# Optimization experiments

Hardware: AMD Instinct MI355X
Metric: run time of the kernel (lower is better)

Reference implementation:

```python
import jax, jax.numpy as jnp
import numpy as np

N = 65536      # total nodes (64 graphs x 1024 nodes)
E = 1048576    # total edges
B = 64         # graphs in the batch
H = 128        # in_dim == hidden_dim
HEAD = 4
EPS = 1e-5


def setup_inputs() -> dict:
    key = jax.random.key(0)
    ks = jax.random.split(key, 16)
    s = 0.02
    return {
        "h": jax.random.normal(ks[0], (N, H), jnp.float32),
        "inter_f": jax.random.normal(ks[1], (B, H), jnp.float32),
        "gamma1": jnp.ones((H,), jnp.float32), "beta1": jnp.zeros((H,), jnp.float32),
        "W1": jax.random.normal(ks[2], (H, H), jnp.float32) * s, "b1": jnp.zeros((H,), jnp.float32),
        "gamma2": jnp.ones((H,), jnp.float32), "beta2": jnp.zeros((H,), jnp.float32),
        "W2": jax.random.normal(ks[3], (H, H), jnp.float32) * s, "b2": jnp.zeros((H,), jnp.float32),
        "Wq": jax.random.normal(ks[4], (HEAD, H, H), jnp.float32) * s,
        "Wk": jax.random.normal(ks[5], (HEAD, H, H), jnp.float32) * s,
        "Wv": jax.random.normal(ks[6], (HEAD, H, H), jnp.float32) * s,
        "Wc": jax.random.normal(ks[7], (HEAD * H, H), jnp.float32) * s,
        "ln_g": jnp.ones((H,), jnp.float32), "ln_b": jnp.zeros((H,), jnp.float32),
        "Wf1": jax.random.normal(ks[8], (H, 2 * H), jnp.float32) * s, "bf1": jnp.zeros((2 * H,), jnp.float32),
        "Wf2": jax.random.normal(ks[9], (2 * H, H), jnp.float32) * s, "bf2": jnp.zeros((H,), jnp.float32),
        "src": jax.random.randint(ks[10], (E,), 0, N, jnp.int32),
        "dst": jax.random.randint(ks[11], (E,), 0, N, jnp.int32),
        "graph_id": (jnp.arange(N) // (N // B)).astype(jnp.int32),
    }


def _bn(x, g, b):
    # BatchNorm1d (training-mode batch statistics, biased var)
    m = x.mean(0)
    v = jnp.mean((x - m) ** 2, 0)
    return (x - m) * jax.lax.rsqrt(v + EPS) * g + b


def _ln(x, g, b):
    m = x.mean(-1, keepdims=True)
    v = jnp.mean((x - m) ** 2, -1, keepdims=True)
    return (x - m) * jax.lax.rsqrt(v + EPS) * g + b


def _gconv(x, W, b, src, dst):
    # dgl GraphConv, norm='both': D_out^{-1/2} gather -> scatter-add -> D_in^{-1/2}, then W, b
    ones_e = jnp.ones((E,), x.dtype)
    dout = jnp.maximum(jax.ops.segment_sum(ones_e, src, num_segments=N), 1.0)
    din = jnp.maximum(jax.ops.segment_sum(ones_e, dst, num_segments=N), 1.0)
    msg = (x * jax.lax.rsqrt(dout)[:, None])[src]            # [E, H] gather
    agg = jax.ops.segment_sum(msg, dst, num_segments=N)      # [N, H] scatter-add
    agg = agg * jax.lax.rsqrt(din)[:, None]
    return agg @ W + b


def _forward(h, inter_f, gamma1, beta1, W1, b1, gamma2, beta2, W2, b2,
             Wq, Wk, Wv, Wc, ln_g, ln_b, Wf1, bf1, Wf2, bf2, src, dst, graph_id):
    # init pooling (mean_nodes)
    counts = jax.ops.segment_sum(jnp.ones((N,), h.dtype), graph_id, num_segments=B)
    init_avg_h = jax.ops.segment_sum(h, graph_id, num_segments=B) / counts[:, None]

    # two residual GraphConv blocks (dropout is identity at inference)
    h1 = h + jax.nn.relu(_gconv(_bn(h, gamma1, beta1), W1, b1, src, dst))
    h2 = h1 + jax.nn.relu(_gconv(_bn(h1, gamma2, beta2), W2, b2, src, dst))

    # broadcast_nodes(inter_f)
    inter_h = inter_f[graph_id]                               # [N, H]

    # transformer_block: per-head q/k/v, per-node scalar att, per-graph segment softmax
    q = jnp.einsum('nd,hdo->hno', h2, Wq)
    k = jnp.einsum('nd,hdo->hno', inter_h, Wk)
    v = jnp.einsum('nd,hdo->hno', h2, Wv)
    att = jnp.sum(q * k, axis=-1) / jnp.sqrt(jnp.float32(1280.0))   # [HEAD, N]
    mx = jax.vmap(lambda a: jax.ops.segment_max(a, graph_id, num_segments=B))(att)  # [HEAD, B]
    e = jnp.exp(att - mx[:, graph_id])
    ssum = jax.vmap(lambda a: jax.ops.segment_sum(a, graph_id, num_segments=B))(e)
    alpha = e / ssum[:, graph_id]                             # segment softmax per head
    tp = v * alpha[..., None]                                 # [HEAD, N, H]
    mo = tp.transpose(1, 0, 2).reshape(N, HEAD * H) @ Wc      # concat heads + project

    x1 = _ln(mo + h2, ln_g, ln_b)
    x2 = _ln(jax.nn.relu(x1 @ Wf1 + bf1) @ Wf2 + bf2 + x1, ln_g, ln_b)

    readout = jax.ops.segment_sum(x2, graph_id, num_segments=B)     # sum_nodes
    return readout, init_avg_h


def reference(h, inter_f, gamma1, beta1, W1, b1, gamma2, beta2, W2, b2,
              Wq, Wk, Wv, Wc, ln_g, ln_b, Wf1, bf1, Wf2, bf2, src, dst, graph_id):
    return _forward(h, inter_f, gamma1, beta1, W1, b1, gamma2, beta2, W2, b2,
                    Wq, Wk, Wv, Wc, ln_g, ln_b, Wf1, bf1, Wf2, bf2, src, dst, graph_id)
```

## Files before the change

kernel.cpp:

```cpp
#include <hip/hip_runtime.h>

#define NN 65536
#define NE 1048576
#define NB 64
#define HD 128
#define HD2 256
#define NHEAD 4
#define NPG 1024
#define BEPS 1e-5f
#define BM 64
#define ESTRIDE 20480

typedef short bf16x8s __attribute__((ext_vector_type(8)));
typedef float f32x4 __attribute__((ext_vector_type(4)));
#define MFMA16(a,b,c) __builtin_amdgcn_mfma_f32_16x16x32_bf16(a,b,c,0,0,0)

__device__ __forceinline__ unsigned short f2bf(float f) {
    union { float f; unsigned int u; } x{f};
    unsigned int r = x.u + 0x7FFFu + ((x.u >> 16) & 1u);
    return (unsigned short)(r >> 16);
}
__device__ __forceinline__ float b2f(unsigned short s) {
    union { unsigned int u; float f; } x{((unsigned int)s) << 16};
    return x.f;
}

__global__ __launch_bounds__(1024) void k_prep_pool(const int* __restrict__ src, const int* __restrict__ dst,
                                                    int* __restrict__ gcurD, int* __restrict__ gcurS,
                                                    unsigned int* __restrict__ dbuck, unsigned short* __restrict__ sbuck,
                                                    const float* __restrict__ h,
                                                    float* __restrict__ psum, float* __restrict__ psq) {
    const int t = threadIdx.x;
    if (blockIdx.x < 64) {
        __shared__ int cntD[64], cntS[64], baseD[64], baseS[64];
        if (t < 64) { cntD[t] = 0; cntS[t] = 0; }
        __syncthreads();
        const int e0 = blockIdx.x * 16384;
        int sv[16], dv[16];
        #pragma unroll
        for (int j = 0; j < 16; ++j) {
            int e = e0 + j * 1024 + t;
            sv[j] = src[e]; dv[j] = dst[e];
            atomicAdd(&cntD[dv[j] >> 10], 1);
            atomicAdd(&cntS[sv[j] >> 10], 1);
        }
        __syncthreads();
        if (t < 64) baseD[t] = atomicAdd(&gcurD[t * 32], cntD[t]);
        else if (t < 128) baseS[t - 64] = atomicAdd(&gcurS[(t - 64) * 32], cntS[t - 64]);
        __syncthreads();
        if (t < 64) { cntD[t] = 0; cntS[t] = 0; }
        __syncthreads();
        #pragma unroll
        for (int j = 0; j < 16; ++j) {
            int gd = dv[j] >> 10;
            int slot = baseD[gd] + atomicAdd(&cntD[gd], 1);
            if (slot < ESTRIDE)
                dbuck[gd * ESTRIDE + slot] = (unsigned)(dv[j] & 1023) | ((unsigned)sv[j] << 10);
            int gs = sv[j] >> 10;
            int slot2 = baseS[gs] + atomicAdd(&cntS[gs], 1);
            if (slot2 < ESTRIDE)
                sbuck[gs * ESTRIDE + slot2] = (unsigned short)(sv[j] & 1023);
        }
    } else {
        __shared__ float ls[1024], lq[1024];
        const int bb = blockIdx.x - 64;
        const int r0 = bb * 256;
        const int c = t & 127, strip8 = t >> 7;
        float s = 0.f, sq = 0.f;
        for (int i = 0; i < 32; ++i) {
            float v = h[(size_t)(r0 + strip8 * 32 + i) * HD + c];
            s += v; sq += v * v;
        }
        ls[t] = s; lq[t] = sq;
        __syncthreads();
        if (t < 128) {
            float ss = 0.f, qq = 0.f;
            #pragma unroll
            for (int k = 0; k < 8; ++k) { ss += ls[t + k * 128]; qq += lq[t + k * 128]; }
            psum[bb * HD + t] = ss;
            psq[bb * HD + t]  = qq;
        }
    }
}

__global__ __launch_bounds__(1024) void k_prep2(const int* __restrict__ gcurD, const int* __restrict__ gcurS,
                                                const unsigned int* __restrict__ dbuck,
                                                const unsigned short* __restrict__ sbuck,
                                                float* __restrict__ din_r, float* __restrict__ dout_r,
                                                int* __restrict__ beg, int* __restrict__ endv,
                                                unsigned short* __restrict__ elist) {
    __shared__ int hist[1024];
    __shared__ int pre[1024];
    const int t = threadIdx.x;
    const int b = blockIdx.x;
    if (b < 64) {
        const int g = b;
        const int n = min(gcurD[g * 32], ESTRIDE);
        const unsigned int* pd = dbuck + g * ESTRIDE;
        hist[t] = 0;
        __syncthreads();
        for (int i = t; i < n; i += 1024) atomicAdd(&hist[pd[i] & 1023], 1);
        __syncthreads();
        const int cnt = hist[t];
        din_r[g * 1024 + t] = rsqrtf((float)max(cnt, 1));
        int x = cnt; pre[t] = x;
        __syncthreads();
        #pragma unroll
        for (int off = 1; off < 1024; off <<= 1) {
            int v = (t >= off) ? pre[t - off] : 0;
            __syncthreads();
            x += v; pre[t] = x;
            __syncthreads();
        }
        const int excl = x - cnt;
        beg[g * 1024 + t]  = g * ESTRIDE + excl;
        endv[g * 1024 + t] = g * ESTRIDE + excl + cnt;
        __syncthreads();
        hist[t] = excl; pre[t] = 0;
        __syncthreads();
        for (int i = t; i < n; i += 1024) {
            unsigned int w = pd[i];
            int dl = w & 1023;
            int r = atomicAdd(&pre[dl], 1);
            elist[g * ESTRIDE + hist[dl] + r] = (unsigned short)(w >> 10);
        }
    } else {
        const int g = b - 64;
        const int m = min(gcurS[g * 32], ESTRIDE);
        const unsigned short* ps = sbuck + g * ESTRIDE;
        hist[t] = 0;
        __syncthreads();
        for (int i = t; i < m; i += 1024) atomicAdd(&hist[ps[i]], 1);
        __syncthreads();
        dout_r[g * 1024 + t] = rsqrtf((float)max(hist[t], 1));
    }
}

__global__ __launch_bounds__(256) void k_sd(const int* __restrict__ beg, const int* __restrict__ endv,
                                            const unsigned short* __restrict__ elist,
                                            const float* __restrict__ dout_r, float* __restrict__ sd) {
    const int node = blockIdx.x * 256 + threadIdx.x;
    const int b0 = beg[node], e0 = endv[node];
    float s = 0.f;
    for (int i = b0; i < e0; ++i) s += dout_r[elist[i]];
    sd[node] = s;
}

__global__ __launch_bounds__(256) void k_pack(const float* __restrict__ x, const float* __restrict__ dout_r,
                                              unsigned short* __restrict__ xr) {
    int idx = blockIdx.x * 256 + threadIdx.x;
    int node = idx >> 4;
    int c8 = (idx & 15) * 8;
    float dr = dout_r[node];
    float4 v0 = *(const float4*)(x + (size_t)node * HD + c8);
    float4 v1 = *(const float4*)(x + (size_t)node * HD + c8 + 4);
    union { uint4 v; unsigned short u[8]; } pk;
    pk.u[0] = f2bf(v0.x * dr); pk.u[1] = f2bf(v0.y * dr);
    pk.u[2] = f2bf(v0.z * dr); pk.u[3] = f2bf(v0.w * dr);
    pk.u[4] = f2bf(v1.x * dr); pk.u[5] = f2bf(v1.y * dr);
    pk.u[6] = f2bf(v1.z * dr); pk.u[7] = f2bf(v1.w * dr);
    *(uint4*)(xr + (size_t)node * HD + c8) = pk.v;
}

__device__ __forceinline__ void dev_prepW(int idx, const float* __restrict__ W,
                                          unsigned short* __restrict__ frag, int O) {
    int l = idx & 63, tt = idx >> 6;
    int ot = O >> 4;
    int c = tt % ot, ks = tt / ot;
    int q = l >> 4, m = l & 15;
    const float* wp = W + (size_t)(ks * 32 + q * 8) * O + c * 16 + m;
    union { uint4 v; unsigned short u[8]; } pk;
    #pragma unroll
    for (int j = 0; j < 8; ++j) pk.u[j] = f2bf(wp[(size_t)j * O]);
    *(uint4*)(frag + (size_t)idx * 8) = pk.v;
}

__global__ __launch_bounds__(256) void k_wprep(const float* __restrict__ W1, const float* __restrict__ W2,
                                               const float* __restrict__ Wf1, const float* __restrict__ Wf2,
                                               const float* __restrict__ interf, const float* __restrict__ Wk,
                                               const float* __restrict__ Wq, const float* __restrict__ Wv,
                                               const float* __restrict__ Wc,
                                               unsigned short* __restrict__ W1f, unsigned short* __restrict__ W2f,
                                               unsigned short* __restrict__ Wf1f, unsigned short* __restrict__ Wf2f,
                                               float* __restrict__ watt, unsigned short* __restrict__ Uf,
                                               const float* __restrict__ psum, const float* __restrict__ psq,
                                               float* __restrict__ out_avg,
                                               float* __restrict__ colsum, float* __restrict__ colsq) {
    const int b = blockIdx.x, t = threadIdx.x;
    if (b < 8)        dev_prepW(b * 256 + t, W1, W1f, 128);
    else if (b < 16)  dev_prepW((b - 8) * 256 + t, W2, W2f, 128);
    else if (b < 32)  dev_prepW((b - 16) * 256 + t, Wf1, Wf1f, 256);
    else if (b < 48)  dev_prepW((b - 32) * 256 + t, Wf2, Wf2f, 128);
    else if (b < 304) {
        int hb = b - 48;
        int hh = hb >> 6, g = hb & 63;
        __shared__ float f[HD];
        __shared__ float kv[HD];
        if (t < HD) f[t] = interf[g * HD + t];
        __syncthreads();
        if (t < HD) {
            const float* Wkh = Wk + (size_t)hh * HD * HD;
            float s = 0.f;
            for (int d = 0; d < HD; ++d) s += f[d] * Wkh[(size_t)d * HD + t];
            kv[t] = s;
        }
        __syncthreads();
        if (t < HD) {
            const float* row = Wq + ((size_t)hh * HD + t) * HD;
            float s2 = 0.f;
            #pragma unroll 4
            for (int o = 0; o < HD; o += 4) {
                float4 w = *(const float4*)(row + o);
                s2 += w.x * kv[o] + w.y * kv[o + 1] + w.z * kv[o + 2] + w.w * kv[o + 3];
            }
            watt[hb * HD + t] = s2 * 0.027950849718747373f;
        }
    } else if (b < 560) {
        int idx = (b - 304) * 256 + t;
        int o = idx & 127;
        int d = (idx >> 7) & 127;
        int hh = idx >> 14;
        const float* wv = Wv + ((size_t)hh * HD + d) * HD;
        const float* wc = Wc + (size_t)(hh * HD) * HD + o;
        float s = 0.f;
        for (int m2 = 0; m2 < HD; ++m2) s += wv[m2] * wc[(size_t)m2 * HD];
        int ks = d >> 5, dd = d & 31, q = dd >> 3, j = dd & 7;
        int c = o >> 4, m = o & 15, l = q * 16 + m;
        Uf[(size_t)((((hh * 4 + ks) * 8 + c) * 64 + l) * 8 + j)] = f2bf(s);
    } else {
        const int col = b - 560;
        __shared__ float ls[256], lq[256];
        ls[t] = psum[t * HD + col];
        lq[t] = psq[t * HD + col];
        __syncthreads();
        if (t < 64) {
            float a4 = ls[4 * t] + ls[4 * t + 1] + ls[4 * t + 2] + ls[4 * t + 3];
            out_avg[t * HD + col] = a4 * (1.0f / NPG);
            float b4 = lq[4 * t] + lq[4 * t + 1] + lq[4 * t + 2] + lq[4 * t + 3];
            float ts = a4, tq = b4;
            #pragma unroll
            for (int mk = 1; mk <= 32; mk <<= 1) {
                ts += __shfl_xor(ts, mk, 64);
                tq += __shfl_xor(tq, mk, 64);
            }
            if (t == 0) { colsum[col] = ts; colsq[col] = tq; }
        }
    }
}

__global__ __launch_bounds__(256) void k_aggregate(const unsigned short* __restrict__ xr,
                                                   const float* __restrict__ din_r, const float* __restrict__ sd,
                                                   const float* __restrict__ colsum, const float* __restrict__ colsq,
                                                   const float* __restrict__ gma, const float* __restrict__ bta,
                                                   const int* __restrict__ beg, const int* __restrict__ endv,
                                                   const unsigned short* __restrict__ elist,
                                                   unsigned short* __restrict__ agg) {
    const int tid = threadIdx.x;
    const int nA = blockIdx.x * 8 + (tid >> 6) * 2;
    const int nB = nA + 1;
    const int c2 = (tid & 63) * 2;
    float m0 = colsum[c2] * (1.0f / NN),     m1 = colsum[c2 + 1] * (1.0f / NN);
    float r0 = rsqrtf(colsq[c2] * (1.0f / NN) - m0 * m0 + BEPS);
    float r1 = rsqrtf(colsq[c2 + 1] * (1.0f / NN) - m1 * m1 + BEPS);
    float sc0 = r0 * gma[c2], sc1 = r1 * gma[c2 + 1];
    float sh0 = bta[c2] - m0 * sc0, sh1 = bta[c2 + 1] - m1 * sc1;

    int iA = beg[nA]; const int eA = endv[nA];
    int iB = beg[nB]; const int eB = endv[nB];
    float a0 = 0.f, a1 = 0.f, b0 = 0.f, b1 = 0.f;
    while (iA + 4 <= eA && iB + 4 <= eB) {
        int sA0 = elist[iA], sA1 = elist[iA + 1], sA2 = elist[iA + 2], sA3 = elist[iA + 3];
        int sB0 = elist[iB], sB1 = elist[iB + 1], sB2 = elist[iB + 2], sB3 = elist[iB + 3];
        unsigned int vA0 = *(const unsigned int*)(xr + (size_t)sA0 * HD + c2);
        unsigned int vB0 = *(const unsigned int*)(xr + (size_t)sB0 * HD + c2);
        unsigned int vA1 = *(const unsigned int*)(xr + (size_t)sA1 * HD + c2);
        unsigned int vB1 = *(const unsigned int*)(xr + (size_t)sB1 * HD + c2);
        unsigned int vA2 = *(const unsigned int*)(xr + (size_t)sA2 * HD + c2);
        unsigned int vB2 = *(const unsigned int*)(xr + (size_t)sB2 * HD + c2);
        unsigned int vA3 = *(const unsigned int*)(xr + (size_t)sA3 * HD + c2);
        unsigned int vB3 = *(const unsigned int*)(xr + (size_t)sB3 * HD + c2);
        a0 += b2f((unsigned short)vA0) + b2f((unsigned short)vA1) + b2f((unsigned short)vA2) + b2f((unsigned short)vA3);
        a1 += b2f((unsigned short)(vA0 >> 16)) + b2f((unsigned short)(vA1 >> 16))
            + b2f((unsigned short)(vA2 >> 16)) + b2f((unsigned short)(vA3 >> 16));
        b0 += b2f((unsigned short)vB0) + b2f((unsigned short)vB1) + b2f((unsigned short)vB2) + b2f((unsigned short)vB3);
        b1 += b2f((unsigned short)(vB0 >> 16)) + b2f((unsigned short)(vB1 >> 16))
            + b2f((unsigned short)(vB2 >> 16)) + b2f((unsigned short)(vB3 >> 16));
        iA += 4; iB += 4;
    }
    for (; iA + 4 <= eA; iA += 4) {
        int s0 = elist[iA], s1 = elist[iA + 1], s2 = elist[iA + 2], s3 = elist[iA + 3];
        unsigned int v0 = *(const unsigned int*)(xr + (size_t)s0 * HD + c2);
        unsigned int v1 = *(const unsigned int*)(xr + (size_t)s1 * HD + c2);
        unsigned int v2 = *(const unsigned int*)(xr + (size_t)s2 * HD + c2);
        unsigned int v3 = *(const unsigned int*)(xr + (size_t)s3 * HD + c2);
        a0 += b2f((unsigned short)v0) + b2f((unsigned short)v1) + b2f((unsigned short)v2) + b2f((unsigned short)v3);
        a1 += b2f((unsigned short)(v0 >> 16)) + b2f((unsigned short)(v1 >> 16))
            + b2f((unsigned short)(v2 >> 16)) + b2f((unsigned short)(v3 >> 16));
    }
    for (; iA < eA; ++iA) {
        unsigned int v = *(const unsigned int*)(xr + (size_t)elist[iA] * HD + c2);
        a0 += b2f((unsigned short)v); a1 += b2f((unsigned short)(v >> 16));
    }
    for (; iB + 4 <= eB; iB += 4) {
        int s0 = elist[iB], s1 = elist[iB + 1], s2 = elist[iB + 2], s3 = elist[iB + 3];
        unsigned int v0 = *(const unsigned int*)(xr + (size_t)s0 * HD + c2);
        unsigned int v1 = *(const unsigned int*)(xr + (size_t)s1 * HD + c2);
        unsigned int v2 = *(const unsigned int*)(xr + (size_t)s2 * HD + c2);
        unsigned int v3 = *(const unsigned int*)(xr + (size_t)s3 * HD + c2);
        b0 += b2f((unsigned short)v0) + b2f((unsigned short)v1) + b2f((unsigned short)v2) + b2f((unsigned short)v3);
        b1 += b2f((unsigned short)(v0 >> 16)) + b2f((unsigned short)(v1 >> 16))
            + b2f((unsigned short)(v2 >> 16)) + b2f((unsigned short)(v3 >> 16));
    }
    for (; iB < eB; ++iB) {
        unsigned int v = *(const unsigned int*)(xr + (size_t)elist[iB] * HD + c2);
        b0 += b2f((unsigned short)v); b1 += b2f((unsigned short)(v >> 16));
    }
    {
        float dn = din_r[nA], sv = sd[nA];
        ushort2 o;
        o.x = f2bf(dn * (a0 * sc0 + sh0 * sv));
        o.y = f2bf(dn * (a1 * sc1 + sh1 * sv));
        *(ushort2*)(agg + (size_t)nA * HD + c2) = o;
    }
    {
        float dn = din_r[nB], sv = sd[nB];
        ushort2 o;
        o.x = f2bf(dn * (b0 * sc0 + sh0 * sv));
        o.y = f2bf(dn * (b1 * sc1 + sh1 * sv));
        *(ushort2*)(agg + (size_t)nB * HD + c2) = o;
    }
}

template<bool SCORES, bool STATS, bool RES32, bool WXR>
__global__ __launch_bounds__(256) void k_gconv_mfma(const unsigned short* __restrict__ agg,
                                                    const unsigned short* __restrict__ Wfrag,
                                                    const float* __restrict__ bias,
                                                    const void* __restrict__ res, unsigned short* __restrict__ outp,
                                                    const float* __restrict__ watt, float* __restrict__ att,
                                                    float* __restrict__ part2s, float* __restrict__ part2q,
                                                    const float* __restrict__ dout_r, unsigned short* __restrict__ xrout) {
    __shared__ float credS[4 * HD];
    __shared__ float credQ[4 * HD];
    const int tid = threadIdx.x;
    const int w = tid >> 6, l = tid & 63, q = l >> 4, m = l & 15;
    const int node = blockIdx.x * BM + w * 16 + m;
    bf16x8s a[4];
    #pragma unroll
    for (int ks = 0; ks < 4; ++ks)
        a[ks] = *(const bf16x8s*)(agg + (size_t)node * HD + ks * 32 + q * 8);
    f32x4 acc[8] = {};
    #pragma unroll
    for (int ks = 0; ks < 4; ++ks) {
        #pragma unroll
        for (int c = 0; c < 8; ++c) {
            bf16x8s b = *(const bf16x8s*)(Wfrag + (size_t)((ks * 8 + c) * 64 + l) * 8);
            acc[c] = MFMA16(b, a[ks], acc[c]);
        }
    }
    float vals[8][4];
    float drv = WXR ? dout_r[node] : 0.f;
    #pragma unroll
    for (int c = 0; c < 8; ++c) {
        const int col = c * 16 + q * 4;
        float4 bv = *(const float4*)(bias + col);
        float rv[4];
        if (RES32) {
            float4 r4 = *(const float4*)((const float*)res + (size_t)node * HD + col);
            rv[0] = r4.x; rv[1] = r4.y; rv[2] = r4.z; rv[3] = r4.w;
        } else {
            ushort4 r4 = *(const ushort4*)((const unsigned short*)res + (size_t)node * HD + col);
            rv[0] = b2f(r4.x); rv[1] = b2f(r4.y); rv[2] = b2f(r4.z); rv[3] = b2f(r4.w);
        }
        vals[c][0] = rv[0] + fmaxf(acc[c][0] + bv.x, 0.f);
        vals[c][1] = rv[1] + fmaxf(acc[c][1] + bv.y, 0.f);
        vals[c][2] = rv[2] + fmaxf(acc[c][2] + bv.z, 0.f);
        vals[c][3] = rv[3] + fmaxf(acc[c][3] + bv.w, 0.f);
        ushort4 o;
        o.x = f2bf(vals[c][0]); o.y = f2bf(vals[c][1]);
        o.z = f2bf(vals[c][2]); o.w = f2bf(vals[c][3]);
        *(ushort4*)(outp + (size_t)node * HD + col) = o;
        if (WXR) {
            ushort4 o2;
            o2.x = f2bf(vals[c][0] * drv); o2.y = f2bf(vals[c][1] * drv);
            o2.z = f2bf(vals[c][2] * drv); o2.w = f2bf(vals[c][3] * drv);
            *(ushort4*)(xrout + (size_t)node * HD + col) = o2;
        }
    }
    if (SCORES) {
        const int g = node >> 10;
        #pragma unroll
        for (int hh = 0; hh < NHEAD; ++hh) {
            const float* wp = watt + ((size_t)(hh * NB + g)) * HD;
            float s = 0.f;
            #pragma unroll
            for (int c = 0; c < 8; ++c) {
                const int col = c * 16 + q * 4;
                float4 wv = *(const float4*)(wp + col);
                s += vals[c][0] * wv.x + vals[c][1] * wv.y + vals[c][2] * wv.z + vals[c][3] * wv.w;
            }
            s += __shfl_xor(s, 16, 64);
            s += __shfl_xor(s, 32, 64);
            if (q == 0) att[(size_t)hh * NN + node] = s;
        }
    }
    if (STATS) {
        #pragma unroll
        for (int c = 0; c < 8; ++c) {
            #pragma unroll
            for (int r = 0; r < 4; ++r) {
                float v = vals[c][r];
                float vq = v * v;
                #pragma unroll
                for (int mk = 1; mk <= 8; mk <<= 1) {
                    v  += __shfl_xor(v, mk, 64);
                    vq += __shfl_xor(vq, mk, 64);
                }
                if (m == 0) {
                    credS[w * HD + c * 16 + q * 4 + r] = v;
                    credQ[w * HD + c * 16 + q * 4 + r] = vq;
                }
            }
        }
        __syncthreads();
        if (tid < HD) {
            part2s[(size_t)blockIdx.x * HD + tid] =
                credS[tid] + credS[HD + tid] + credS[2 * HD + tid] + credS[3 * HD + tid];
            part2q[(size_t)blockIdx.x * HD + tid] =
                credQ[tid] + credQ[HD + tid] + credQ[2 * HD + tid] + credQ[3 * HD + tid];
        }
    }
}

__global__ __launch_bounds__(256) void k_red2(const float* __restrict__ part2s, const float* __restrict__ part2q,
                                              float* __restrict__ colsum, float* __restrict__ colsq) {
    __shared__ float ws[8];
    const int col = blockIdx.x, t = threadIdx.x;
    float s = 0.f, sq = 0.f;
    #pragma unroll
    for (int k = 0; k < 4; ++k) {
        s  += part2s[(size_t)(t + k * 256) * HD + col];
        sq += part2q[(size_t)(t + k * 256) * HD + col];
    }
    #pragma unroll
    for (int mk = 1; mk <= 32; mk <<= 1) {
        s  += __shfl_xor(s, mk, 64);
        sq += __shfl_xor(sq, mk, 64);
    }
    if ((t & 63) == 0) { ws[(t >> 6) * 2] = s; ws[(t >> 6) * 2 + 1] = sq; }
    __syncthreads();
    if (t == 0) colsum[col] = ws[0] + ws[2] + ws[4] + ws[6];
    if (t == 1) colsq[col]  = ws[1] + ws[3] + ws[5] + ws[7];
}

__global__ __launch_bounds__(256) void k_segsoftmax(const float* __restrict__ att, float* __restrict__ alpha) {
    const int hh = blockIdx.x >> 6, g = blockIdx.x & 63;
    const int t = threadIdx.x;
    const float* a = att + (size_t)hh * NN + g * NPG;
    float* al = alpha + (size_t)hh * NN + g * NPG;
    float v[4]; float mx = -1e30f;
    #pragma unroll
    for (int i = 0; i < 4; ++i) { v[i] = a[t + i * 256]; mx = fmaxf(mx, v[i]); }
    #pragma unroll
    for (int m = 32; m > 0; m >>= 1) mx = fmaxf(mx, __shfl_xor(mx, m, 64));
    __shared__ float redm[4], reds[4];
    if ((t & 63) == 0) redm[t >> 6] = mx;
    __syncthreads();
    mx = fmaxf(fmaxf(redm[0], redm[1]), fmaxf(redm[2], redm[3]));
    float s = 0.f;
    #pragma unroll
    for (int i = 0; i < 4; ++i) { v[i] = __expf(v[i] - mx); s += v[i]; }
    #pragma unroll
    for (int m = 32; m > 0; m >>= 1) s += __shfl_xor(s, m, 64);
    if ((t & 63) == 0) reds[t >> 6] = s;
    __syncthreads();
    s = reds[0] + reds[1] + reds[2] + reds[3];
    float inv = 1.f / s;
    #pragma unroll
    for (int i = 0; i < 4; ++i) al[t + i * 256] = v[i] * inv;
}

__global__ __launch_bounds__(256) void k_mo_x1(const unsigned short* __restrict__ h2b,
                                               const unsigned short* __restrict__ Ufrag,
                                               const float* __restrict__ alpha,
                                               const float* __restrict__ lng, const float* __restrict__ lnb,
                                               unsigned short* __restrict__ x1b) {
    const int tid = threadIdx.x;
    const int w = tid >> 6, l = tid & 63, q = l >> 4, m = l & 15;
    const int node = blockIdx.x * BM + w * 16 + m;
    bf16x8s a[4];
    #pragma unroll
    for (int ks = 0; ks < 4; ++ks)
        a[ks] = *(const bf16x8s*)(h2b + (size_t)node * HD + ks * 32 + q * 8);
    f32x4 mo[8] = {};
    #pragma unroll
    for (int hh = 0; hh < 4; ++hh) {
        f32x4 acc[8] = {};
        #pragma unroll
        for (int ks = 0; ks < 4; ++ks) {
            #pragma unroll
            for (int c = 0; c < 8; ++c) {
                bf16x8s b = *(const bf16x8s*)(Ufrag + (size_t)(((hh * 4 + ks) * 8 + c) * 64 + l) * 8);
                acc[c] = MFMA16(b, a[ks], acc[c]);
            }
        }
        float al = alpha[(size_t)hh * NN + node];
        #pragma unroll
        for (int c = 0; c < 8; ++c) {
            mo[c][0] += al * acc[c][0];
            mo[c][1] += al * acc[c][1];
            mo[c][2] += al * acc[c][2];
            mo[c][3] += al * acc[c][3];
        }
    }
    float vals[8][4]; float s = 0.f, sq = 0.f;
    #pragma unroll
    for (int c = 0; c < 8; ++c) {
        const int col = c * 16 + q * 4;
        ushort4 hv = *(const ushort4*)(h2b + (size_t)node * HD + col);
        vals[c][0] = mo[c][0] + b2f(hv.x);
        vals[c][1] = mo[c][1] + b2f(hv.y);
        vals[c][2] = mo[c][2] + b2f(hv.z);
        vals[c][3] = mo[c][3] + b2f(hv.w);
        #pragma unroll
        for (int r = 0; r < 4; ++r) { s += vals[c][r]; sq += vals[c][r] * vals[c][r]; }
    }
    s  += __shfl_xor(s, 16, 64);  s  += __shfl_xor(s, 32, 64);
    sq += __shfl_xor(sq, 16, 64); sq += __shfl_xor(sq, 32, 64);
    float mean = s * (1.f / HD);
    float var  = sq * (1.f / HD) - mean * mean;
    float rstd = rsqrtf(var + BEPS);
    #pragma unroll
    for (int c = 0; c < 8; ++c) {
        const int col = c * 16 + q * 4;
        float4 gv = *(const float4*)(lng + col);
        float4 bv = *(const float4*)(lnb + col);
        ushort4 o;
        o.x = f2bf((vals[c][0] - mean) * rstd * gv.x + bv.x);
        o.y = f2bf((vals[c][1] - mean) * rstd * gv.y + bv.y);
        o.z = f2bf((vals[c][2] - mean) * rstd * gv.z + bv.z);
        o.w = f2bf((vals[c][3] - mean) * rstd * gv.w + bv.w);
        *(ushort4*)(x1b + (size_t)node * HD + col) = o;
    }
}

__global__ __launch_bounds__(256) void k_ffn1_mfma(const unsigned short* __restrict__ x1b,
                                                   const unsigned short* __restrict__ Wfrag,
                                                   const float* __restrict__ bias,
                                                   unsigned short* __restrict__ mid) {
    const int tid = threadIdx.x;
    const int w = tid >> 6, l = tid & 63, q = l >> 4, m = l & 15;
    const int node = blockIdx.x * BM + w * 16 + m;
    bf16x8s a[4];
    #pragma unroll
    for (int ks = 0; ks < 4; ++ks)
        a[ks] = *(const bf16x8s*)(x1b + (size_t)node * HD + ks * 32 + q * 8);
    f32x4 acc[16] = {};
    #pragma unroll
    for (int ks = 0; ks < 4; ++ks) {
        #pragma unroll
        for (int c = 0; c < 16; ++c) {
            bf16x8s b = *(const bf16x8s*)(Wfrag + (size_t)((ks * 16 + c) * 64 + l) * 8);
            acc[c] = MFMA16(b, a[ks], acc[c]);
        }
    }
    #pragma unroll
    for (int c = 0; c < 16; ++c) {
        const int col = c * 16 + q * 4;
        float4 bv = *(const float4*)(bias + col);
        ushort4 o;
        o.x = f2bf(fmaxf(acc[c][0] + bv.x, 0.f));
        o.y = f2bf(fmaxf(acc[c][1] + bv.y, 0.f));
        o.z = f2bf(fmaxf(acc[c][2] + bv.z, 0.f));
        o.w = f2bf(fmaxf(acc[c][3] + bv.w, 0.f));
        *(ushort4*)(mid + (size_t)node * HD2 + col) = o;
    }
}

__global__ __launch_bounds__(256) void k_ffn2_mfma(const unsigned short* __restrict__ mid,
                                                   const unsigned short* __restrict__ Wfrag,
                                                   const float* __restrict__ bias,
                                                   const unsigned short* __restrict__ x1b,
                                                   const float* __restrict__ lng, const float* __restrict__ lnb,
                                                   float* __restrict__ rpart) {
    __shared__ float cred[4 * HD];
    const int tid = threadIdx.x;
    const int w = tid >> 6, l = tid & 63, q = l >> 4, m = l & 15;
    const int node = blockIdx.x * BM + w * 16 + m;
    bf16x8s a[8];
    #pragma unroll
    for (int ks = 0; ks < 8; ++ks)
        a[ks] = *(const bf16x8s*)(mid + (size_t)node * HD2 + ks * 32 + q * 8);
    f32x4 acc[8] = {};
    #pragma unroll
    for (int ks = 0; ks < 8; ++ks) {
        #pragma unroll
        for (int c = 0; c < 8; ++c) {
            bf16x8s b = *(const bf16x8s*)(Wfrag + (size_t)((ks * 8 + c) * 64 + l) * 8);
            acc[c] = MFMA16(b, a[ks], acc[c]);
        }
    }
    float vals[8][4]; float s = 0.f, sq = 0.f;
    #pragma unroll
    for (int c = 0; c < 8; ++c) {
        const int col = c * 16 + q * 4;
        float4 bv = *(const float4*)(bias + col);
        ushort4 xv = *(const ushort4*)(x1b + (size_t)node * HD + col);
        vals[c][0] = acc[c][0] + bv.x + b2f(xv.x);
        vals[c][1] = acc[c][1] + bv.y + b2f(xv.y);
        vals[c][2] = acc[c][2] + bv.z + b2f(xv.z);
        vals[c][3] = acc[c][3] + bv.w + b2f(xv.w);
        #pragma unroll
        for (int r = 0; r < 4; ++r) { s += vals[c][r]; sq += vals[c][r] * vals[c][r]; }
    }
    s  += __shfl_xor(s, 16, 64);  s  += __shfl_xor(s, 32, 64);
    sq += __shfl_xor(sq, 16, 64); sq += __shfl_xor(sq, 32, 64);
    float mean = s * (1.f / HD);
    float var  = sq * (1.f / HD) - mean * mean;
    float rstd = rsqrtf(var + BEPS);
    #pragma unroll
    for (int c = 0; c < 8; ++c) {
        const int col = c * 16 + q * 4;
        float4 gv = *(const float4*)(lng + col);
        float4 bv = *(const float4*)(lnb + col);
        float4 o;
        o.x = (vals[c][0] - mean) * rstd * gv.x + bv.x;
        o.y = (vals[c][1] - mean) * rstd * gv.y + bv.y;
        o.z = (vals[c][2] - mean) * rstd * gv.z + bv.z;
        o.w = (vals[c][3] - mean) * rstd * gv.w + bv.w;
        #pragma unroll
        for (int mk = 1; mk <= 8; mk <<= 1) {
            o.x += __shfl_xor(o.x, mk, 64);
            o.y += __shfl_xor(o.y, mk, 64);
            o.z += __shfl_xor(o.z, mk, 64);
            o.w += __shfl_xor(o.w, mk, 64);
        }
        if (m == 0) *(float4*)(cred + w * HD + col) = o;
    }
    __syncthreads();
    if (tid < HD)
        rpart[(size_t)blockIdx.x * HD + tid] =
            cred[tid] + cred[HD + tid] + cred[2 * HD + tid] + cred[3 * HD + tid];
}

__global__ __launch_bounds__(256) void k_redout(const float* __restrict__ rpart, float* __restrict__ outp) {
    __shared__ float ls[256];
    const int g = blockIdx.x, t = threadIdx.x;
    const int c = t & 127, half = t >> 7;
    float s = 0.f;
    #pragma unroll
    for (int k = 0; k < 8; ++k)
        s += rpart[(size_t)(g * 16 + half * 8 + k) * HD + c];
    ls[t] = s;
    __syncthreads();
    if (t < 128) outp[g * HD + t] = ls[t] + ls[t + 128];
}

extern "C" void kernel_launch(void* const* d_in, const int* in_sizes, int n_in,
                              void* d_out, int out_size, void* d_ws, size_t ws_size,
                              hipStream_t stream) {
    (void)in_sizes; (void)n_in; (void)out_size;
    const float* h      = (const float*)d_in[0];
    const float* interf = (const float*)d_in[1];
    const float* gamma1 = (const float*)d_in[2];
    const float* beta1  = (const float*)d_in[3];
    const float* W1     = (const float*)d_in[4];
    const float* b1     = (const float*)d_in[5];
    const float* gamma2 = (const float*)d_in[6];
    const float* beta2  = (const float*)d_in[7];
    const float* W2     = (const float*)d_in[8];
    const float* b2     = (const float*)d_in[9];
    const float* Wq     = (const float*)d_in[10];
    const float* Wk     = (const float*)d_in[11];
    const float* Wv     = (const float*)d_in[12];
    const float* Wc     = (const float*)d_in[13];
    const float* ln_g   = (const float*)d_in[14];
    const float* ln_b   = (const float*)d_in[15];
    const float* Wf1    = (const float*)d_in[16];
    const float* bf1    = (const float*)d_in[17];
    const float* Wf2    = (const float*)d_in[18];
    const float* bf2    = (const float*)d_in[19];
    const int*   src    = (const int*)d_in[20];
    const int*   dst    = (const int*)d_in[21];

    float* out = (float*)d_out;
    float* R1 = (float*)d_ws;
    float* R2 = R1 + 8388608;
    float* R3 = R2 + 8388608;
    float* aux = R3 + 8388608;

    unsigned int*   dbuck = (unsigned int*)R1;
    unsigned short* sbuck = (unsigned short*)(R1 + 1310720);
    unsigned short* h1b   = (unsigned short*)R1;
    unsigned short* x1b   = (unsigned short*)R1;
    unsigned short* elist = (unsigned short*)R2;
    unsigned short* h2b   = (unsigned short*)R2;
    float* rpart  = R2 + 4194304;
    float* part2s = R2 + 4325376;
    float* part2q = R2 + 4456448;
    float* psum   = R2 + 4587520;
    float* psq    = R2 + 4620288;
    unsigned short* xr   = (unsigned short*)R3;
    unsigned short* aggb = (unsigned short*)(R3 + 4194304);
    float* att    = R3;
    float* alpha  = R3 + 262144;
    unsigned short* mid = (unsigned short*)R3;

    float* dout_r  = aux;
    float* din_r   = aux + 65536;
    float* colsum1 = aux + 131072;
    float* colsq1  = aux + 131200;
    float* colsum2 = aux + 131328;
    float* colsq2  = aux + 131456;
    int*   gcurD   = (int*)(aux + 131584);
    int*   gcurS   = (int*)(aux + 133632);
    float* watt    = aux + 135680;
    int*   beg     = (int*)(aux + 168448);
    int*   endv    = (int*)(aux + 233984);
    float* sd      = aux + 299520;
    unsigned short* W1f  = (unsigned short*)(aux + 365056);
    unsigned short* W2f  = (unsigned short*)(aux + 373248);
    unsigned short* Wf1f = (unsigned short*)(aux + 381440);
    unsigned short* Wf2f = (unsigned short*)(aux + 397824);
    unsigned short* Uf   = (unsigned short*)(aux + 414208);

    if (ws_size < (size_t)(25165824 + 446976) * 4) return;

    hipMemsetAsync(gcurD, 0, 4096 * sizeof(int), stream);

    k_prep_pool<<<320, 1024, 0, stream>>>(src, dst, gcurD, gcurS, dbuck, sbuck, h, psum, psq);
    k_prep2<<<128, 1024, 0, stream>>>(gcurD, gcurS, dbuck, sbuck, din_r, dout_r, beg, endv, elist);
    k_sd<<<256, 256, 0, stream>>>(beg, endv, elist, dout_r, sd);
    k_pack<<<4096, 256, 0, stream>>>(h, dout_r, xr);
    k_wprep<<<688, 256, 0, stream>>>(W1, W2, Wf1, Wf2, interf, Wk, Wq, Wv, Wc,
                                     W1f, W2f, Wf1f, Wf2f, watt, Uf,
                                     psum, psq, out + 8192, colsum1, colsq1);

    k_aggregate<<<8192, 256, 0, stream>>>(xr, din_r, sd, colsum1, colsq1, gamma1, beta1,
                                          beg, endv, elist, aggb);
    k_gconv_mfma<false, true, true, true><<<1024, 256, 0, stream>>>(aggb, W1f, b1, h, h1b,
                                                                    nullptr, nullptr, part2s, part2q,
                                                                    dout_r, xr);
    k_red2<<<128, 256, 0, stream>>>(part2s, part2q, colsum2, colsq2);

    k_aggregate<<<8192, 256, 0, stream>>>(xr, din_r, sd, colsum2, colsq2, gamma2, beta2,
                                          beg, endv, elist, aggb);
    k_gconv_mfma<true, false, false, false><<<1024, 256, 0, stream>>>(aggb, W2f, b2, h1b, h2b,
                                                                      watt, att, nullptr, nullptr,
                                                                      nullptr, nullptr);

    k_segsoftmax<<<256, 256, 0, stream>>>(att, alpha);
    k_mo_x1<<<1024, 256, 0, stream>>>(h2b, Uf, alpha, ln_g, ln_b, x1b);
    k_ffn1_mfma<<<1024, 256, 0, stream>>>(x1b, Wf1f, bf1, mid);
    k_ffn2_mfma<<<1024, 256, 0, stream>>>(mid, Wf2f, bf2, x1b, ln_g, ln_b, rpart);
    k_redout<<<64, 256, 0, stream>>>(rpart, out);
}
```

Baseline: 285.6 us.

## Split aggregation edges across lane groups with 16-byte gathers; merge sd and pack kernels

```diff
diff --git a/kernel.cpp b/kernel.cpp
--- a/kernel.cpp
+++ b/kernel.cpp
@@ -136,30 +136,31 @@
     }
 }
 
-__global__ __launch_bounds__(256) void k_sd(const int* __restrict__ beg, const int* __restrict__ endv,
-                                            const unsigned short* __restrict__ elist,
-                                            const float* __restrict__ dout_r, float* __restrict__ sd) {
-    const int node = blockIdx.x * 256 + threadIdx.x;
-    const int b0 = beg[node], e0 = endv[node];
-    float s = 0.f;
-    for (int i = b0; i < e0; ++i) s += dout_r[elist[i]];
-    sd[node] = s;
-}
-
-__global__ __launch_bounds__(256) void k_pack(const float* __restrict__ x, const float* __restrict__ dout_r,
-                                              unsigned short* __restrict__ xr) {
-    int idx = blockIdx.x * 256 + threadIdx.x;
-    int node = idx >> 4;
-    int c8 = (idx & 15) * 8;
-    float dr = dout_r[node];
-    float4 v0 = *(const float4*)(x + (size_t)node * HD + c8);
-    float4 v1 = *(const float4*)(x + (size_t)node * HD + c8 + 4);
-    union { uint4 v; unsigned short u[8]; } pk;
-    pk.u[0] = f2bf(v0.x * dr); pk.u[1] = f2bf(v0.y * dr);
-    pk.u[2] = f2bf(v0.z * dr); pk.u[3] = f2bf(v0.w * dr);
-    pk.u[4] = f2bf(v1.x * dr); pk.u[5] = f2bf(v1.y * dr);
-    pk.u[6] = f2bf(v1.z * dr); pk.u[7] = f2bf(v1.w * dr);
-    *(uint4*)(xr + (size_t)node * HD + c8) = pk.v;
+__global__ __launch_bounds__(256) void k_sdpack(const float* __restrict__ x, const float* __restrict__ dout_r,
+                                                unsigned short* __restrict__ xr,
+                                                const int* __restrict__ beg, const int* __restrict__ endv,
+                                                const unsigned short* __restrict__ elist,
+                                                float* __restrict__ sd) {
+    if (blockIdx.x < 4096) {
+        int idx = blockIdx.x * 256 + threadIdx.x;
+        int node = idx >> 4;
+        int c8 = (idx & 15) * 8;
+        float dr = dout_r[node];
+        float4 v0 = *(const float4*)(x + (size_t)node * HD + c8);
+        float4 v1 = *(const float4*)(x + (size_t)node * HD + c8 + 4);
+        union { uint4 v; unsigned short u[8]; } pk;
+        pk.u[0] = f2bf(v0.x * dr); pk.u[1] = f2bf(v0.y * dr);
+        pk.u[2] = f2bf(v0.z * dr); pk.u[3] = f2bf(v0.w * dr);
+        pk.u[4] = f2bf(v1.x * dr); pk.u[5] = f2bf(v1.y * dr);
+        pk.u[6] = f2bf(v1.z * dr); pk.u[7] = f2bf(v1.w * dr);
+        *(uint4*)(xr + (size_t)node * HD + c8) = pk.v;
+    } else {
+        const int node = (blockIdx.x - 4096) * 256 + threadIdx.x;
+        const int b0 = beg[node], e0 = endv[node];
+        float s = 0.f;
+        for (int i = b0; i < e0; ++i) s += dout_r[elist[i]];
+        sd[node] = s;
+    }
 }
 
 __device__ __forceinline__ void dev_prepW(int idx, const float* __restrict__ W,
@@ -256,78 +257,49 @@
                                                    const unsigned short* __restrict__ elist,
                                                    unsigned short* __restrict__ agg) {
     const int tid = threadIdx.x;
-    const int nA = blockIdx.x * 8 + (tid >> 6) * 2;
-    const int nB = nA + 1;
-    const int c2 = (tid & 63) * 2;
-    float m0 = colsum[c2] * (1.0f / NN),     m1 = colsum[c2 + 1] * (1.0f / NN);
-    float r0 = rsqrtf(colsq[c2] * (1.0f / NN) - m0 * m0 + BEPS);
-    float r1 = rsqrtf(colsq[c2 + 1] * (1.0f / NN) - m1 * m1 + BEPS);
-    float sc0 = r0 * gma[c2], sc1 = r1 * gma[c2 + 1];
-    float sh0 = bta[c2] - m0 * sc0, sh1 = bta[c2 + 1] - m1 * sc1;
-
-    int iA = beg[nA]; const int eA = endv[nA];
-    int iB = beg[nB]; const int eB = endv[nB];
-    float a0 = 0.f, a1 = 0.f, b0 = 0.f, b1 = 0.f;
-    while (iA + 4 <= eA && iB + 4 <= eB) {
-        int sA0 = elist[iA], sA1 = elist[iA + 1], sA2 = elist[iA + 2], sA3 = elist[iA + 3];
-        int sB0 = elist[iB], sB1 = elist[iB + 1], sB2 = elist[iB + 2], sB3 = elist[iB + 3];
-        unsigned int vA0 = *(const unsigned int*)(xr + (size_t)sA0 * HD + c2);
-        unsigned int vB0 = *(const unsigned int*)(xr + (size_t)sB0 * HD + c2);
-        unsigned int vA1 = *(const unsigned int*)(xr + (size_t)sA1 * HD + c2);
-        unsigned int vB1 = *(const unsigned int*)(xr + (size_t)sB1 * HD + c2);
-        unsigned int vA2 = *(const unsigned int*)(xr + (size_t)sA2 * HD + c2);
-        unsigned int vB2 = *(const unsigned int*)(xr + (size_t)sB2 * HD + c2);
-        unsigned int vA3 = *(const unsigned int*)(xr + (size_t)sA3 * HD + c2);
-        unsigned int vB3 = *(const unsigned int*)(xr + (size_t)sB3 * HD + c2);
-        a0 += b2f((unsigned short)vA0) + b2f((unsigned short)vA1) + b2f((unsigned short)vA2) + b2f((unsigned short)vA3);
-        a1 += b2f((unsigned short)(vA0 >> 16)) + b2f((unsigned short)(vA1 >> 16))
-            + b2f((unsigned short)(vA2 >> 16)) + b2f((unsigned short)(vA3 >> 16));
-        b0 += b2f((unsigned short)vB0) + b2f((unsigned short)vB1) + b2f((unsigned short)vB2) + b2f((unsigned short)vB3);
-        b1 += b2f((unsigned short)(vB0 >> 16)) + b2f((unsigned short)(vB1 >> 16))
-            + b2f((unsigned short)(vB2 >> 16)) + b2f((unsigned short)(vB3 >> 16));
-        iA += 4; iB += 4;
-    }
-    for (; iA + 4 <= eA; iA += 4) {
-        int s0 = elist[iA], s1 = elist[iA + 1], s2 = elist[iA + 2], s3 = elist[iA + 3];
-        unsigned int v0 = *(const unsigned int*)(xr + (size_t)s0 * HD + c2);
-        unsigned int v1 = *(const unsigned int*)(xr + (size_t)s1 * HD + c2);
-        unsigned int v2 = *(const unsigned int*)(xr + (size_t)s2 * HD + c2);
-        unsigned int v3 = *(const unsigned int*)(xr + (size_t)s3 * HD + c2);
-        a0 += b2f((unsigned short)v0) + b2f((unsigned short)v1) + b2f((unsigned short)v2) + b2f((unsigned short)v3);
-        a1 += b2f((unsigned short)(v0 >> 16)) + b2f((unsigned short)(v1 >> 16))
-            + b2f((unsigned short)(v2 >> 16)) + b2f((unsigned short)(v3 >> 16));
-    }
-    for (; iA < eA; ++iA) {
-        unsigned int v = *(const unsigned int*)(xr + (size_t)elist[iA] * HD + c2);
-        a0 += b2f((unsigned short)v); a1 += b2f((unsigned short)(v >> 16));
-    }
-    for (; iB + 4 <= eB; iB += 4) {
-        int s0 = elist[iB], s1 = elist[iB + 1], s2 = elist[iB + 2], s3 = elist[iB + 3];
-        unsigned int v0 = *(const unsigned int*)(xr + (size_t)s0 * HD + c2);
-        unsigned int v1 = *(const unsigned int*)(xr + (size_t)s1 * HD + c2);
-        unsigned int v2 = *(const unsigned int*)(xr + (size_t)s2 * HD + c2);
-        unsigned int v3 = *(const unsigned int*)(xr + (size_t)s3 * HD + c2);
-        b0 += b2f((unsigned short)v0) + b2f((unsigned short)v1) + b2f((unsigned short)v2) + b2f((unsigned short)v3);
-        b1 += b2f((unsigned short)(v0 >> 16)) + b2f((unsigned short)(v1 >> 16))
-            + b2f((unsigned short)(v2 >> 16)) + b2f((unsigned short)(v3 >> 16));
-    }
-    for (; iB < eB; ++iB) {
-        unsigned int v = *(const unsigned int*)(xr + (size_t)elist[iB] * HD + c2);
-        b0 += b2f((unsigned short)v); b1 += b2f((unsigned short)(v >> 16));
-    }
-    {
-        float dn = din_r[nA], sv = sd[nA];
-        ushort2 o;
-        o.x = f2bf(dn * (a0 * sc0 + sh0 * sv));
-        o.y = f2bf(dn * (a1 * sc1 + sh1 * sv));
-        *(ushort2*)(agg + (size_t)nA * HD + c2) = o;
-    }
-    {
-        float dn = din_r[nB], sv = sd[nB];
-        ushort2 o;
-        o.x = f2bf(dn * (b0 * sc0 + sh0 * sv));
-        o.y = f2bf(dn * (b1 * sc1 + sh1 * sv));
-        *(ushort2*)(agg + (size_t)nB * HD + c2) = o;
+    const int node = blockIdx.x * 4 + (tid >> 6);
+    const int lane = tid & 63;
+    const int grp = lane >> 4;
+    const int gl = lane & 15;
+    const int c8 = gl * 8;
+    const int b0 = beg[node], e0 = endv[node];
+    float a[8] = {};
+    int i = b0 + grp;
+    for (; i + 12 < e0; i += 16) {
+        int s0 = elist[i], s1 = elist[i + 4], s2 = elist[i + 8], s3 = elist[i + 12];
+        union { uint4 v; unsigned short u[8]; } r0, r1, r2, r3;
+        r0.v = *(const uint4*)(xr + (size_t)s0 * HD + c8);
+        r1.v = *(const uint4*)(xr + (size_t)s1 * HD + c8);
+        r2.v = *(const uint4*)(xr + (size_t)s2 * HD + c8);
+        r3.v = *(const uint4*)(xr + (size_t)s3 * HD + c8);
+        #pragma unroll
+        for (int j = 0; j < 8; ++j)
+            a[j] += b2f(r0.u[j]) + b2f(r1.u[j]) + b2f(r2.u[j]) + b2f(r3.u[j]);
+    }
+    for (; i < e0; i += 4) {
+        int s = elist[i];
+        union { uint4 v; unsigned short u[8]; } r;
+        r.v = *(const uint4*)(xr + (size_t)s * HD + c8);
+        #pragma unroll
+        for (int j = 0; j < 8; ++j) a[j] += b2f(r.u[j]);
+    }
+    #pragma unroll
+    for (int j = 0; j < 8; ++j) {
+        a[j] += __shfl_xor(a[j], 16, 64);
+        a[j] += __shfl_xor(a[j], 32, 64);
+    }
+    if (grp == 0) {
+        float dn = din_r[node], sv = sd[node];
+        union { uint4 v; unsigned short u[8]; } o;
+        #pragma unroll
+        for (int j = 0; j < 8; ++j) {
+            float mj = colsum[c8 + j] * (1.0f / NN);
+            float rj = rsqrtf(colsq[c8 + j] * (1.0f / NN) - mj * mj + BEPS);
+            float scj = rj * gma[c8 + j];
+            float shj = bta[c8 + j] - mj * scj;
+            o.u[j] = f2bf(dn * (a[j] * scj + shj * sv));
+        }
+        *(uint4*)(agg + (size_t)node * HD + c8) = o.v;
     }
 }
 
@@ -729,21 +701,20 @@
 
     k_prep_pool<<<320, 1024, 0, stream>>>(src, dst, gcurD, gcurS, dbuck, sbuck, h, psum, psq);
     k_prep2<<<128, 1024, 0, stream>>>(gcurD, gcurS, dbuck, sbuck, din_r, dout_r, beg, endv, elist);
-    k_sd<<<256, 256, 0, stream>>>(beg, endv, elist, dout_r, sd);
-    k_pack<<<4096, 256, 0, stream>>>(h, dout_r, xr);
+    k_sdpack<<<4352, 256, 0, stream>>>(h, dout_r, xr, beg, endv, elist, sd);
     k_wprep<<<688, 256, 0, stream>>>(W1, W2, Wf1, Wf2, interf, Wk, Wq, Wv, Wc,
                                      W1f, W2f, Wf1f, Wf2f, watt, Uf,
                                      psum, psq, out + 8192, colsum1, colsq1);
 
-    k_aggregate<<<8192, 256, 0, stream>>>(xr, din_r, sd, colsum1, colsq1, gamma1, beta1,
-                                          beg, endv, elist, aggb);
+    k_aggregate<<<16384, 256, 0, stream>>>(xr, din_r, sd, colsum1, colsq1, gamma1, beta1,
+                                           beg, endv, elist, aggb);
     k_gconv_mfma<false, true, true, true><<<1024, 256, 0, stream>>>(aggb, W1f, b1, h, h1b,
                                                                     nullptr, nullptr, part2s, part2q,
                                                                     dout_r, xr);
     k_red2<<<128, 256, 0, stream>>>(part2s, part2q, colsum2, colsq2);
 
-    k_aggregate<<<8192, 256, 0, stream>>>(xr, din_r, sd, colsum2, colsq2, gamma2, beta2,
-                                          beg, endv, elist, aggb);
+    k_aggregate<<<16384, 256, 0, stream>>>(xr, din_r, sd, colsum2, colsq2, gamma2, beta2,
+                                           beg, endv, elist, aggb);
     k_gconv_mfma<true, false, false, false><<<1024, 256, 0, stream>>>(aggb, W2f, b2, h1b, h2b,
                                                                       watt, att, nullptr, nullptr,
                                                                       nullptr, nullptr);
```

Result: slower. 291.7 us (+2.1%).
